# Optimization experiments

Measured on AMD Instinct MI355X. Metric: run time of the kernel, lower is better.

## Reference

```python
import jax, jax.numpy as jnp
import numpy as np

B, N_STEPS, N_TUMBLES = 512, 20000, 64
RATE_01 = RATE_10 = RATE_02 = RATE_20 = 1e-3
SPEED_0, SPEED_1 = 1e-3, 5e-3
DT = 0.01
PA_MU, PA_SIG = 0.0, 0.1   # planar cauchy
NP_MU, NP_SIG = 0.0, 0.5   # nonplanar cauchy


def _normalise(v):
    return v / jnp.linalg.norm(v, axis=-1, keepdims=True)


def _orthogonalise(v, u):
    return v - (jnp.sum(v * u, -1, keepdims=True) / jnp.sum(u * u, -1, keepdims=True)) * u


def _cauchy_angles(u, mu, sigma):
    # inverse-CDF cauchy sample, nan/inf -> 0, fmod pi (matches torch semantics)
    a = mu + sigma * jnp.tan(np.pi * (u - 0.5))
    a = jnp.where(jnp.isfinite(a), a, 0.0)
    return jnp.fmod(a, np.pi)


def _skew(u):  # (B,3) -> (B,3,3), [u]_x
    z = jnp.zeros_like(u[:, 0])
    return jnp.stack([
        jnp.stack([z, -u[:, 2], u[:, 1]], -1),
        jnp.stack([u[:, 2], z, -u[:, 0]], -1),
        jnp.stack([-u[:, 1], u[:, 0], z], -1)], -2)


def _rodrigues(u, ang):  # rotation about unit axis u by ang, per batch
    I = jnp.eye(3, dtype=u.dtype)
    c = jnp.cos(ang)[:, None, None]
    s = jnp.sin(ang)[:, None, None]
    return c * I + s * _skew(u) + (1.0 - c) * jnp.einsum('bi,bj->bij', u, u)


def setup_inputs() -> dict:
    key = jax.random.key(0)
    k = jax.random.split(key, 6)
    return {
        'x0': jnp.zeros((B, 3), jnp.float32),
        'v0': jax.random.uniform(k[0], (B, 3), jnp.float32),
        'v1': jax.random.uniform(k[1], (B, 3), jnp.float32),
        'r0': jax.random.uniform(k[2], (B, N_STEPS), jnp.float32),
        'r1': jax.random.uniform(k[3], (B, N_STEPS), jnp.float32),
        'u_planar': jax.random.uniform(k[4], (B, N_TUMBLES), jnp.float32),
        'u_nonplanar': jax.random.uniform(k[5], (B, N_TUMBLES), jnp.float32),
        'T': 200,
    }


def reference(x0, v0, v1, r0, r1, u_planar, u_nonplanar, T):
    b, n_steps = r0.shape

    # ---- three-state Markov chain over time (sequential) ----
    def state_step(s, rt):
        r0t, r1t = rt
        from0 = jnp.where(r0t < RATE_01, 1, jnp.where(r0t > 1.0 - RATE_02, 2, 0))
        from1 = jnp.where(r1t < RATE_10, 0, 1)
        from2 = jnp.where(r1t < RATE_20, 0, 1)
        ns = jnp.where(s == 0, from0, jnp.where(s == 1, from1, from2))
        return ns, ns

    s0 = jnp.zeros((b,), jnp.int32)
    _, states_t = jax.lax.scan(state_step, s0, (r0.T, r1.T))
    states = states_t.T  # (B, n_steps)

    # ---- initial orthonormal frame ----
    e0 = _normalise(v0)
    e1 = _normalise(_orthogonalise(v1, e0))
    e2 = _normalise(jnp.cross(e0, e1))

    # ---- tumble rotations (sequential over tumble events) ----
    pa = _cauchy_angles(u_planar, PA_MU, PA_SIG)      # (B, cap)
    npa = _cauchy_angles(u_nonplanar, NP_MU, NP_SIG)  # (B, cap)

    def rot_step(frames, angs):
        e0, e1, e2 = frames
        a_p, a_n = angs
        Rp = _rodrigues(e2, a_p)  # planar: rotate about e2
        e0 = _normalise(jnp.einsum('bij,bj->bi', Rp, e0))
        e1 = _normalise(jnp.einsum('bij,bj->bi', Rp, e1))
        e1 = _normalise(_orthogonalise(e1, e0))
        e2 = _normalise(jnp.cross(e0, e1))
        Rn = _rodrigues(e1, a_n)  # nonplanar: rotate about e1
        e0 = _normalise(jnp.einsum('bij,bj->bi', Rn, e0))
        e1 = _normalise(_orthogonalise(e1, e0))
        e2 = _normalise(jnp.cross(e0, e1))
        return (e0, e1, e2), e0

    _, e0_hist = jax.lax.scan(rot_step, (e0, e1, e2), (pa.T, npa.T))
    e0s = jnp.concatenate([e0[:, None, :], jnp.transpose(e0_hist, (1, 0, 2))], axis=1)  # (B, cap+1, 3)

    # ---- trajectory: per-step velocity = active frame * speed(state), 0 during tumbles ----
    tumble = (states == 2).at[:, 0].set(False)  # loop in original starts at step 1
    c = jnp.cumsum(tumble.astype(jnp.int32), axis=1)
    # original: k=0; at each tumble e0=e0s[:,k]; k+=1 => after m tumbles active frame is e0s[:, max(m-1,0)]
    idx = jnp.clip(c - 1, 0, pa.shape[1])
    frames = jnp.take_along_axis(e0s, idx[..., None], axis=1)  # (B, n_steps, 3)
    speed = jnp.where(states == 1, SPEED_1, SPEED_0).astype(frames.dtype)[..., None]
    vel = jnp.where(tumble[..., None], 0.0, frames * speed)
    vel = vel.at[:, 0, :].set(x0)  # e0_exp[:,0] = x
    X = jnp.cumsum(vel, axis=1)  # (B, n_steps, 3)
    return X
```

## Files before the change

### kernel.cpp

```cpp
#include <hip/hip_runtime.h>
#include <math.h>
#include <stdint.h>

#define NB 512
#define NT 20000
#define CAP 64
#define CHUNK 100
#define NC 200
#define NWORDS ((NB * NT) / 32)

static_assert(CHUNK * NC == NT, "chunking must cover all steps");
static_assert((NB * NT) % 64 == 0, "pack wave alignment");
static_assert(NT % 32 == 0, "b*NT word-aligned");

#define PI_F 3.14159265358979323846f

__device__ __forceinline__ float3 f3(float x, float y, float z) { return make_float3(x, y, z); }

__device__ __forceinline__ float3 norm3(float3 v) {
    float n = sqrtf(v.x * v.x + v.y * v.y + v.z * v.z);
    return f3(v.x / n, v.y / n, v.z / n);
}
__device__ __forceinline__ float3 cross3(float3 a, float3 b) {
    return f3(a.y * b.z - a.z * b.y, a.z * b.x - a.x * b.z, a.x * b.y - a.y * b.x);
}
__device__ __forceinline__ float dot3(float3 a, float3 b) { return a.x * b.x + a.y * b.y + a.z * b.z; }
__device__ __forceinline__ float3 orth3(float3 v, float3 u) {
    float d = dot3(v, u) / dot3(u, u);
    return f3(v.x - d * u.x, v.y - d * u.y, v.z - d * u.z);
}
__device__ __forceinline__ float3 rotv(float3 u, float c, float s, float3 v) {
    float3 cv = cross3(u, v);
    float du = dot3(u, v) * (1.0f - c);
    return f3(c * v.x + s * cv.x + du * u.x,
              c * v.y + s * cv.y + du * u.y,
              c * v.z + s * cv.z + du * u.z);
}

__device__ __forceinline__ float cauchy_ang(float u, float sigma) {
    float x = PI_F * (u - 0.5f);
    float t = (float)tan((double)x);
    float a = sigma * t;
    if (!isfinite(a)) a = 0.0f;
    return fmodf(a, PI_F);
}

__global__ __launch_bounds__(256) void k_angles(const float* __restrict__ up, const float* __restrict__ un,
                                                float* __restrict__ trig) {
    int tid = blockIdx.x * 256 + threadIdx.x;
    int k = tid >> 9, b = tid & (NB - 1);
    float ap = cauchy_ang(up[b * CAP + k], 0.1f);
    float an = cauchy_ang(un[b * CAP + k], 0.5f);
    ((float4*)trig)[tid] = make_float4(cosf(ap), sinf(ap), cosf(an), sinf(an));
}

__global__ __launch_bounds__(64) void k_chain(const float* __restrict__ v0, const float* __restrict__ v1,
                                              const float* __restrict__ trig, float* __restrict__ e0s) {
    int b = blockIdx.x * 64 + threadIdx.x;
    if (b >= NB) return;
    float3 a0 = f3(v0[b * 3], v0[b * 3 + 1], v0[b * 3 + 2]);
    float3 a1 = f3(v1[b * 3], v1[b * 3 + 1], v1[b * 3 + 2]);
    float3 e0 = norm3(a0);
    float3 e1 = norm3(orth3(a1, e0));
    float3 e2 = norm3(cross3(e0, e1));
    float* o = e0s + (size_t)b * (CAP + 1) * 3;
    o[0] = e0.x; o[1] = e0.y; o[2] = e0.z;
    for (int k = 0; k < CAP; k++) {
        float4 t4 = ((const float4*)trig)[k * NB + b];
        float cp = t4.x, sp = t4.y, cn = t4.z, sn = t4.w;
        float3 e0r = rotv(e2, cp, sp, e0);
        float3 e1r = rotv(e2, cp, sp, e1);
        e0 = norm3(e0r);
        e1 = norm3(e1r);
        e1 = norm3(orth3(e1, e0));
        e2 = norm3(cross3(e0, e1));
        e0 = norm3(rotv(e1, cn, sn, e0));
        e1 = norm3(orth3(e1, e0));
        e2 = norm3(cross3(e0, e1));
        o[(k + 1) * 3] = e0.x; o[(k + 1) * 3 + 1] = e0.y; o[(k + 1) * 3 + 2] = e0.z;
    }
}

__global__ __launch_bounds__(256) void k_pack(const float* __restrict__ r0, const float* __restrict__ r1,
                                              uint32_t* __restrict__ p0, uint32_t* __restrict__ p1,
                                              uint32_t* __restrict__ pf) {
    int g = blockIdx.x * 256 + threadIdx.x;
    float a = r0[g], d = r1[g];
    int f0 = (a < 1e-3f) ? 1 : ((a > (1.0f - 1e-3f)) ? 2 : 0);
    int f1 = (d < 1e-3f) ? 0 : 1;
    uint64_t b0 = __ballot(f0 & 1);
    uint64_t b1 = __ballot((f0 >> 1) & 1);
    uint64_t bf = __ballot(f1);
    if ((threadIdx.x & 63) == 0) {
        int w = g >> 6;
        ((uint64_t*)p0)[w] = b0;
        ((uint64_t*)p1)[w] = b1;
        ((uint64_t*)pf)[w] = bf;
    }
}

__device__ __forceinline__ void load100(const uint32_t* __restrict__ p, int w0, int off, uint32_t r[4]) {
    uint32_t q0 = p[w0], q1 = p[w0 + 1], q2 = p[w0 + 2], q3 = p[w0 + 3], q4 = p[w0 + 4];
    r[0] = __builtin_amdgcn_alignbit(q1, q0, off);
    r[1] = __builtin_amdgcn_alignbit(q2, q1, off);
    r[2] = __builtin_amdgcn_alignbit(q3, q2, off);
    r[3] = __builtin_amdgcn_alignbit(q4, q3, off);
}

#define GETB(R, t) ((R[(t) >> 5] >> ((t) & 31)) & 1u)

__global__ __launch_bounds__(512) void k_summary(const uint32_t* __restrict__ p0, const uint32_t* __restrict__ p1,
                                                 const uint32_t* __restrict__ pf, uint32_t* __restrict__ comb) {
    int c = blockIdx.x, b = threadIdx.x;
    int g0 = b * NT + c * CHUNK;
    uint32_t R0[4], R1[4], RF[4];
    load100(p0, g0 >> 5, g0 & 31, R0);
    load100(p1, g0 >> 5, g0 & 31, R1);
    load100(pf, g0 >> 5, g0 & 31, RF);
    int s0 = 0, s1 = 1, s2 = 2, c0 = 0, c1 = 0, c2 = 0;
#pragma unroll
    for (int t = 0; t < CHUNK; t++) {
        int f0 = (int)(GETB(R0, t) | (GETB(R1, t) << 1));
        int f1 = (int)GETB(RF, t);
        s0 = (s0 == 0) ? f0 : f1;
        s1 = (s1 == 0) ? f0 : f1;
        s2 = (s2 == 0) ? f0 : f1;
        bool skip = (c == 0) && (t == 0);
        c0 += (s0 == 2 && !skip);
        c1 += (s1 == 2 && !skip);
        c2 += (s2 == 2 && !skip);
    }
    comb[c * NB + b] = (uint32_t)(s0 | (s1 << 2) | (s2 << 4) | (c0 << 8) | (c1 << 16) | (c2 << 24));
}

__global__ void k_scan_state(const uint32_t* __restrict__ comb, uint32_t* __restrict__ entry) {
    int b = blockIdx.x * blockDim.x + threadIdx.x;
    if (b >= NB) return;
    uint32_t s = 0, C = 0;
#pragma unroll 4
    for (int c = 0; c < NC; c++) {
        uint32_t m = comb[c * NB + b];
        entry[c * NB + b] = s | (C << 2);
        C += (m >> (8 + 8 * s)) & 0xFF;
        s = (m >> (2 * s)) & 3;
    }
}

template <int MODE>
__global__ __launch_bounds__(256) void k_walk(const uint32_t* __restrict__ p0, const uint32_t* __restrict__ p1,
                                              const uint32_t* __restrict__ pf,
                                              const float* __restrict__ x0, const float* __restrict__ e0s,
                                              const uint32_t* __restrict__ entry,
                                              const float* __restrict__ epos,
                                              float* __restrict__ cvel, float* __restrict__ out) {
    __shared__ float se[(CAP + 1) * 3];
    int b = blockIdx.x, c = threadIdx.x;
    for (int i = threadIdx.x; i < (CAP + 1) * 3; i += blockDim.x)
        se[i] = e0s[(size_t)b * (CAP + 1) * 3 + i];
    __syncthreads();
    if (c >= NC) return;
    int g0 = b * NT + c * CHUNK;
    uint32_t R0[4], R1[4], RF[4];
    load100(p0, g0 >> 5, g0 & 31, R0);
    load100(p1, g0 >> 5, g0 & 31, R1);
    load100(pf, g0 >> 5, g0 & 31, RF);
    uint32_t e = entry[c * NB + b];
    int s = (int)(e & 3);
    int C = (int)(e >> 2);
    float px = 0.f, py = 0.f, pz = 0.f;
    if (MODE == 1) {
        const float* pp = epos + (size_t)(c * NB + b) * 3;
        px = pp[0]; py = pp[1]; pz = pp[2];
    }
    float* op = out + (size_t)(b * NT + c * CHUNK) * 3;
#pragma unroll
    for (int t = 0; t < CHUNK; t++) {
        int f0 = (int)(GETB(R0, t) | (GETB(R1, t) << 1));
        int f1 = (int)GETB(RF, t);
        s = (s == 0) ? f0 : f1;
        float vx, vy, vz;
        if (c == 0 && t == 0) {
            vx = x0[b * 3]; vy = x0[b * 3 + 1]; vz = x0[b * 3 + 2];
        } else if (s == 2) {
            C++;
            vx = 0.f; vy = 0.f; vz = 0.f;
        } else {
            int idx = C - 1;
            idx = idx < 0 ? 0 : (idx > CAP ? CAP : idx);
            float spd = (s == 1) ? 5e-3f : 1e-3f;
            vx = se[idx * 3] * spd; vy = se[idx * 3 + 1] * spd; vz = se[idx * 3 + 2] * spd;
        }
        px += vx; py += vy; pz += vz;
        if (MODE == 1) {
            op[t * 3] = px; op[t * 3 + 1] = py; op[t * 3 + 2] = pz;
        }
    }
    if (MODE == 0) {
        float* cv = cvel + (size_t)(c * NB + b) * 3;
        cv[0] = px; cv[1] = py; cv[2] = pz;
    }
}

__global__ void k_scan_pos(const float* __restrict__ cvel, float* __restrict__ epos) {
    int b = blockIdx.x * blockDim.x + threadIdx.x;
    if (b >= NB) return;
    float px = 0.f, py = 0.f, pz = 0.f;
#pragma unroll 4
    for (int c = 0; c < NC; c++) {
        float* ep = epos + (size_t)(c * NB + b) * 3;
        ep[0] = px; ep[1] = py; ep[2] = pz;
        const float* cv = cvel + (size_t)(c * NB + b) * 3;
        px += cv[0]; py += cv[1]; pz += cv[2];
    }
}

extern "C" void kernel_launch(void* const* d_in, const int* in_sizes, int n_in,
                              void* d_out, int out_size, void* d_ws, size_t ws_size,
                              hipStream_t stream) {
    const float* x0 = (const float*)d_in[0];
    const float* v0 = (const float*)d_in[1];
    const float* v1 = (const float*)d_in[2];
    const float* r0 = (const float*)d_in[3];
    const float* r1 = (const float*)d_in[4];
    const float* up = (const float*)d_in[5];
    const float* un = (const float*)d_in[6];
    float* out = (float*)d_out;

    char* w = (char*)d_ws;
    float* trig = (float*)w;       w += (size_t)NB * CAP * 4 * sizeof(float);
    float* e0s = (float*)w;        w += (size_t)NB * (CAP + 1) * 3 * sizeof(float);
    uint32_t* p0 = (uint32_t*)w;   w += (size_t)(NWORDS + 16) * 4;
    uint32_t* p1 = (uint32_t*)w;   w += (size_t)(NWORDS + 16) * 4;
    uint32_t* pf = (uint32_t*)w;   w += (size_t)(NWORDS + 16) * 4;
    uint32_t* comb = (uint32_t*)w; w += (size_t)NC * NB * 4;
    uint32_t* entry = (uint32_t*)w; w += (size_t)NC * NB * 4;
    float* cvel = (float*)w;       w += (size_t)NC * NB * 3 * sizeof(float);
    float* epos = (float*)w;       w += (size_t)NC * NB * 3 * sizeof(float);

    k_angles<<<dim3(NB * CAP / 256), dim3(256), 0, stream>>>(up, un, trig);
    k_chain<<<dim3(NB / 64), dim3(64), 0, stream>>>(v0, v1, trig, e0s);
    k_pack<<<dim3(NB * NT / 256), dim3(256), 0, stream>>>(r0, r1, p0, p1, pf);
    k_summary<<<dim3(NC), dim3(NB), 0, stream>>>(p0, p1, pf, comb);
    k_scan_state<<<dim3(2), dim3(256), 0, stream>>>(comb, entry);
    k_walk<0><<<dim3(NB), dim3(256), 0, stream>>>(p0, p1, pf, x0, e0s, entry, nullptr, cvel, nullptr);
    k_scan_pos<<<dim3(2), dim3(256), 0, stream>>>(cvel, epos);
    k_walk<1><<<dim3(NB), dim3(256), 0, stream>>>(p0, p1, pf, x0, e0s, entry, epos, nullptr, out);
}
```

Baseline: 401.5 us.

## Fuse pack, state scan, and position scan into one per-row kernel

Replaces the six-kernel pipeline (bit-packing, chunk summaries, serial state scan, two walks, serial position scan) with a single kernel that has one block per batch row. Each block packs the flags into shared memory and computes the three-state chunk summaries. It then runs Hillis-Steele scans in shared memory for state/count composition and for partial positions. Output writes are vectorised as float4 per four steps. This removes kernel launches, global round-trips and the slow single-thread serial scans over chunks. The cost is block-level barriers and a recomputation pass, and it changes the chunk size to 80.

```diff
diff --git a/kernel.cpp b/kernel.cpp
--- a/kernel.cpp
+++ b/kernel.cpp
@@ -5,13 +5,12 @@
 #define NB 512
 #define NT 20000
 #define CAP 64
-#define CHUNK 100
-#define NC 200
-#define NWORDS ((NB * NT) / 32)
+#define CHUNK 80
+#define NC 250
+#define CPAD 21
 
 static_assert(CHUNK * NC == NT, "chunking must cover all steps");
-static_assert((NB * NT) % 64 == 0, "pack wave alignment");
-static_assert(NT % 32 == 0, "b*NT word-aligned");
+static_assert(CHUNK % 4 == 0, "byte-packing needs 4 | CHUNK");
 
 #define PI_F 3.14159265358979323846f
 
@@ -81,136 +80,186 @@
     }
 }
 
-__global__ __launch_bounds__(256) void k_pack(const float* __restrict__ r0, const float* __restrict__ r1,
-                                              uint32_t* __restrict__ p0, uint32_t* __restrict__ p1,
-                                              uint32_t* __restrict__ pf) {
-    int g = blockIdx.x * 256 + threadIdx.x;
-    float a = r0[g], d = r1[g];
-    int f0 = (a < 1e-3f) ? 1 : ((a > (1.0f - 1e-3f)) ? 2 : 0);
-    int f1 = (d < 1e-3f) ? 0 : 1;
-    uint64_t b0 = __ballot(f0 & 1);
-    uint64_t b1 = __ballot((f0 >> 1) & 1);
-    uint64_t bf = __ballot(f1);
-    if ((threadIdx.x & 63) == 0) {
-        int w = g >> 6;
-        ((uint64_t*)p0)[w] = b0;
-        ((uint64_t*)p1)[w] = b1;
-        ((uint64_t*)pf)[w] = bf;
-    }
-}
-
-__device__ __forceinline__ void load100(const uint32_t* __restrict__ p, int w0, int off, uint32_t r[4]) {
-    uint32_t q0 = p[w0], q1 = p[w0 + 1], q2 = p[w0 + 2], q3 = p[w0 + 3], q4 = p[w0 + 4];
-    r[0] = __builtin_amdgcn_alignbit(q1, q0, off);
-    r[1] = __builtin_amdgcn_alignbit(q2, q1, off);
-    r[2] = __builtin_amdgcn_alignbit(q3, q2, off);
-    r[3] = __builtin_amdgcn_alignbit(q4, q3, off);
-}
-
-#define GETB(R, t) ((R[(t) >> 5] >> ((t) & 31)) & 1u)
-
-__global__ __launch_bounds__(512) void k_summary(const uint32_t* __restrict__ p0, const uint32_t* __restrict__ p1,
-                                                 const uint32_t* __restrict__ pf, uint32_t* __restrict__ comb) {
-    int c = blockIdx.x, b = threadIdx.x;
-    int g0 = b * NT + c * CHUNK;
-    uint32_t R0[4], R1[4], RF[4];
-    load100(p0, g0 >> 5, g0 & 31, R0);
-    load100(p1, g0 >> 5, g0 & 31, R1);
-    load100(pf, g0 >> 5, g0 & 31, RF);
-    int s0 = 0, s1 = 1, s2 = 2, c0 = 0, c1 = 0, c2 = 0;
-#pragma unroll
-    for (int t = 0; t < CHUNK; t++) {
-        int f0 = (int)(GETB(R0, t) | (GETB(R1, t) << 1));
-        int f1 = (int)GETB(RF, t);
-        s0 = (s0 == 0) ? f0 : f1;
-        s1 = (s1 == 0) ? f0 : f1;
-        s2 = (s2 == 0) ? f0 : f1;
-        bool skip = (c == 0) && (t == 0);
-        c0 += (s0 == 2 && !skip);
-        c1 += (s1 == 2 && !skip);
-        c2 += (s2 == 2 && !skip);
-    }
-    comb[c * NB + b] = (uint32_t)(s0 | (s1 << 2) | (s2 << 4) | (c0 << 8) | (c1 << 16) | (c2 << 24));
-}
-
-__global__ void k_scan_state(const uint32_t* __restrict__ comb, uint32_t* __restrict__ entry) {
-    int b = blockIdx.x * blockDim.x + threadIdx.x;
-    if (b >= NB) return;
-    uint32_t s = 0, C = 0;
-#pragma unroll 4
-    for (int c = 0; c < NC; c++) {
-        uint32_t m = comb[c * NB + b];
-        entry[c * NB + b] = s | (C << 2);
-        C += (m >> (8 + 8 * s)) & 0xFF;
-        s = (m >> (2 * s)) & 3;
-    }
-}
-
-template <int MODE>
-__global__ __launch_bounds__(256) void k_walk(const uint32_t* __restrict__ p0, const uint32_t* __restrict__ p1,
-                                              const uint32_t* __restrict__ pf,
-                                              const float* __restrict__ x0, const float* __restrict__ e0s,
-                                              const uint32_t* __restrict__ entry,
-                                              const float* __restrict__ epos,
-                                              float* __restrict__ cvel, float* __restrict__ out) {
+__device__ __forceinline__ uint4 comb2(uint4 A, uint4 B) {
+    uint4 R;
+    R.x = 0;
+    {
+        unsigned ms = A.x & 3u;
+        unsigned mf = (B.x >> (2u * ms)) & 3u;
+        R.x |= mf;
+        unsigned cB = (ms == 0u) ? B.y : ((ms == 1u) ? B.z : B.w);
+        R.y = A.y + cB;
+    }
+    {
+        unsigned ms = (A.x >> 2) & 3u;
+        unsigned mf = (B.x >> (2u * ms)) & 3u;
+        R.x |= mf << 2;
+        unsigned cB = (ms == 0u) ? B.y : ((ms == 1u) ? B.z : B.w);
+        R.z = A.z + cB;
+    }
+    {
+        unsigned ms = (A.x >> 4) & 3u;
+        unsigned mf = (B.x >> (2u * ms)) & 3u;
+        R.x |= mf << 4;
+        unsigned cB = (ms == 0u) ? B.y : ((ms == 1u) ? B.z : B.w);
+        R.w = A.w + cB;
+    }
+    return R;
+}
+
+#define DECODE(dw, t, f0, f1)                                        \
+    {                                                                \
+        uint32_t by_ = (dw[(t) >> 2] >> (((t) & 3) * 8)) & 0xFFu;    \
+        f0 = (int)(by_ & 3u);                                        \
+        f1 = (int)((by_ >> 2) & 1u);                                 \
+    }
+
+__global__ __launch_bounds__(256) void k_row(const float* __restrict__ r0, const float* __restrict__ r1,
+                                             const float* __restrict__ x0, const float* __restrict__ e0s,
+                                             float* __restrict__ out) {
+    __shared__ uint32_t dec[NC * CPAD];
     __shared__ float se[(CAP + 1) * 3];
-    int b = blockIdx.x, c = threadIdx.x;
-    for (int i = threadIdx.x; i < (CAP + 1) * 3; i += blockDim.x)
+    __shared__ uint4 S[NC];
+    __shared__ float Px[NC], Py[NC], Pz[NC];
+
+    int b = blockIdx.x, tid = threadIdx.x;
+
+    for (int i = tid; i < (CAP + 1) * 3; i += 256)
         se[i] = e0s[(size_t)b * (CAP + 1) * 3 + i];
+
+    const float4* q0 = (const float4*)(r0 + (size_t)b * NT);
+    const float4* q1 = (const float4*)(r1 + (size_t)b * NT);
+    for (int T = tid; T < NT / 4; T += 256) {
+        float4 a = q0[T], d = q1[T];
+        float ra[4] = {a.x, a.y, a.z, a.w};
+        float rd[4] = {d.x, d.y, d.z, d.w};
+        uint32_t w = 0;
+#pragma unroll
+        for (int j = 0; j < 4; j++) {
+            int f0 = (ra[j] < 1e-3f) ? 1 : ((ra[j] > (1.0f - 1e-3f)) ? 2 : 0);
+            int f1 = (rd[j] < 1e-3f) ? 0 : 1;
+            w |= (uint32_t)(f0 | (f1 << 2)) << (8 * j);
+        }
+        int t0 = T * 4;
+        int c = t0 / CHUNK;
+        int o = t0 - c * CHUNK;
+        dec[c * CPAD + (o >> 2)] = w;
+    }
     __syncthreads();
-    if (c >= NC) return;
-    int g0 = b * NT + c * CHUNK;
-    uint32_t R0[4], R1[4], RF[4];
-    load100(p0, g0 >> 5, g0 & 31, R0);
-    load100(p1, g0 >> 5, g0 & 31, R1);
-    load100(pf, g0 >> 5, g0 & 31, RF);
-    uint32_t e = entry[c * NB + b];
-    int s = (int)(e & 3);
-    int C = (int)(e >> 2);
-    float px = 0.f, py = 0.f, pz = 0.f;
-    if (MODE == 1) {
-        const float* pp = epos + (size_t)(c * NB + b) * 3;
-        px = pp[0]; py = pp[1]; pz = pp[2];
-    }
-    float* op = out + (size_t)(b * NT + c * CHUNK) * 3;
-#pragma unroll
-    for (int t = 0; t < CHUNK; t++) {
-        int f0 = (int)(GETB(R0, t) | (GETB(R1, t) << 1));
-        int f1 = (int)GETB(RF, t);
-        s = (s == 0) ? f0 : f1;
-        float vx, vy, vz;
-        if (c == 0 && t == 0) {
-            vx = x0[b * 3]; vy = x0[b * 3 + 1]; vz = x0[b * 3 + 2];
-        } else if (s == 2) {
-            C++;
-            vx = 0.f; vy = 0.f; vz = 0.f;
-        } else {
-            int idx = C - 1;
-            idx = idx < 0 ? 0 : (idx > CAP ? CAP : idx);
-            float spd = (s == 1) ? 5e-3f : 1e-3f;
-            vx = se[idx * 3] * spd; vy = se[idx * 3 + 1] * spd; vz = se[idx * 3 + 2] * spd;
-        }
-        px += vx; py += vy; pz += vz;
-        if (MODE == 1) {
-            op[t * 3] = px; op[t * 3 + 1] = py; op[t * 3 + 2] = pz;
-        }
-    }
-    if (MODE == 0) {
-        float* cv = cvel + (size_t)(c * NB + b) * 3;
-        cv[0] = px; cv[1] = py; cv[2] = pz;
-    }
-}
-
-__global__ void k_scan_pos(const float* __restrict__ cvel, float* __restrict__ epos) {
-    int b = blockIdx.x * blockDim.x + threadIdx.x;
-    if (b >= NB) return;
-    float px = 0.f, py = 0.f, pz = 0.f;
-#pragma unroll 4
-    for (int c = 0; c < NC; c++) {
-        float* ep = epos + (size_t)(c * NB + b) * 3;
-        ep[0] = px; ep[1] = py; ep[2] = pz;
-        const float* cv = cvel + (size_t)(c * NB + b) * 3;
-        px += cv[0]; py += cv[1]; pz += cv[2];
+
+    int c = tid;
+    uint32_t dw[CHUNK / 4];
+    if (c < NC) {
+#pragma unroll
+        for (int wi = 0; wi < CHUNK / 4; wi++) dw[wi] = dec[c * CPAD + wi];
+        int s0 = 0, s1 = 1, s2 = 2, c0 = 0, c1 = 0, c2 = 0;
+#pragma unroll
+        for (int t = 0; t < CHUNK; t++) {
+            int f0, f1;
+            DECODE(dw, t, f0, f1);
+            s0 = (s0 == 0) ? f0 : f1;
+            s1 = (s1 == 0) ? f0 : f1;
+            s2 = (s2 == 0) ? f0 : f1;
+            bool skip = (c == 0) && (t == 0);
+            c0 += (s0 == 2 && !skip);
+            c1 += (s1 == 2 && !skip);
+            c2 += (s2 == 2 && !skip);
+        }
+        S[c] = make_uint4((unsigned)(s0 | (s1 << 2) | (s2 << 4)),
+                          (unsigned)c0, (unsigned)c1, (unsigned)c2);
+    }
+    __syncthreads();
+
+    for (int off = 1; off < NC; off <<= 1) {
+        uint4 prev;
+        bool act = (c < NC) && (c >= off);
+        if (act) prev = S[c - off];
+        __syncthreads();
+        if (act) S[c] = comb2(prev, S[c]);
+        __syncthreads();
+    }
+
+    int es = 0;
+    uint32_t eC = 0;
+    if (c > 0 && c < NC) {
+        uint4 E = S[c - 1];
+        es = (int)(E.x & 3u);
+        eC = E.y;
+    }
+
+    float xx0 = x0[b * 3], xy0 = x0[b * 3 + 1], xz0 = x0[b * 3 + 2];
+
+    if (c < NC) {
+        int s = es;
+        uint32_t C = eC;
+        float px = 0.f, py = 0.f, pz = 0.f;
+#pragma unroll
+        for (int t = 0; t < CHUNK; t++) {
+            int f0, f1;
+            DECODE(dw, t, f0, f1);
+            s = (s == 0) ? f0 : f1;
+            float vx, vy, vz;
+            if (c == 0 && t == 0) {
+                vx = xx0; vy = xy0; vz = xz0;
+            } else if (s == 2) {
+                C++;
+                vx = 0.f; vy = 0.f; vz = 0.f;
+            } else {
+                int idx = (int)C - 1;
+                idx = idx < 0 ? 0 : (idx > CAP ? CAP : idx);
+                float spd = (s == 1) ? 5e-3f : 1e-3f;
+                vx = se[idx * 3] * spd; vy = se[idx * 3 + 1] * spd; vz = se[idx * 3 + 2] * spd;
+            }
+            px += vx; py += vy; pz += vz;
+        }
+        Px[c] = px; Py[c] = py; Pz[c] = pz;
+    }
+    __syncthreads();
+
+    for (int off = 1; off < NC; off <<= 1) {
+        float ax, ay, az;
+        bool act = (c < NC) && (c >= off);
+        if (act) { ax = Px[c - off]; ay = Py[c - off]; az = Pz[c - off]; }
+        __syncthreads();
+        if (act) { Px[c] += ax; Py[c] += ay; Pz[c] += az; }
+        __syncthreads();
+    }
+
+    if (c < NC) {
+        float px = 0.f, py = 0.f, pz = 0.f;
+        if (c > 0) { px = Px[c - 1]; py = Py[c - 1]; pz = Pz[c - 1]; }
+        int s = es;
+        uint32_t C = eC;
+        float* op = out + ((size_t)b * NT + (size_t)c * CHUNK) * 3;
+#pragma unroll
+        for (int g = 0; g < CHUNK / 4; g++) {
+            float buf[12];
+#pragma unroll
+            for (int j = 0; j < 4; j++) {
+                int t = g * 4 + j;
+                int f0, f1;
+                DECODE(dw, t, f0, f1);
+                s = (s == 0) ? f0 : f1;
+                float vx, vy, vz;
+                if (c == 0 && t == 0) {
+                    vx = xx0; vy = xy0; vz = xz0;
+                } else if (s == 2) {
+                    C++;
+                    vx = 0.f; vy = 0.f; vz = 0.f;
+                } else {
+                    int idx = (int)C - 1;
+                    idx = idx < 0 ? 0 : (idx > CAP ? CAP : idx);
+                    float spd = (s == 1) ? 5e-3f : 1e-3f;
+                    vx = se[idx * 3] * spd; vy = se[idx * 3 + 1] * spd; vz = se[idx * 3 + 2] * spd;
+                }
+                px += vx; py += vy; pz += vz;
+                buf[j * 3] = px; buf[j * 3 + 1] = py; buf[j * 3 + 2] = pz;
+            }
+            float4* o4 = (float4*)(op + g * 12);
+            o4[0] = make_float4(buf[0], buf[1], buf[2], buf[3]);
+            o4[1] = make_float4(buf[4], buf[5], buf[6], buf[7]);
+            o4[2] = make_float4(buf[8], buf[9], buf[10], buf[11]);
+        }
     }
 }
 
@@ -227,22 +276,10 @@
     float* out = (float*)d_out;
 
     char* w = (char*)d_ws;
-    float* trig = (float*)w;       w += (size_t)NB * CAP * 4 * sizeof(float);
-    float* e0s = (float*)w;        w += (size_t)NB * (CAP + 1) * 3 * sizeof(float);
-    uint32_t* p0 = (uint32_t*)w;   w += (size_t)(NWORDS + 16) * 4;
-    uint32_t* p1 = (uint32_t*)w;   w += (size_t)(NWORDS + 16) * 4;
-    uint32_t* pf = (uint32_t*)w;   w += (size_t)(NWORDS + 16) * 4;
-    uint32_t* comb = (uint32_t*)w; w += (size_t)NC * NB * 4;
-    uint32_t* entry = (uint32_t*)w; w += (size_t)NC * NB * 4;
-    float* cvel = (float*)w;       w += (size_t)NC * NB * 3 * sizeof(float);
-    float* epos = (float*)w;       w += (size_t)NC * NB * 3 * sizeof(float);
+    float* trig = (float*)w;  w += (size_t)NB * CAP * 4 * sizeof(float);
+    float* e0s = (float*)w;   w += (size_t)NB * (CAP + 1) * 3 * sizeof(float);
 
     k_angles<<<dim3(NB * CAP / 256), dim3(256), 0, stream>>>(up, un, trig);
     k_chain<<<dim3(NB / 64), dim3(64), 0, stream>>>(v0, v1, trig, e0s);
-    k_pack<<<dim3(NB * NT / 256), dim3(256), 0, stream>>>(r0, r1, p0, p1, pf);
-    k_summary<<<dim3(NC), dim3(NB), 0, stream>>>(p0, p1, pf, comb);
-    k_scan_state<<<dim3(2), dim3(256), 0, stream>>>(comb, entry);
-    k_walk<0><<<dim3(NB), dim3(256), 0, stream>>>(p0, p1, pf, x0, e0s, entry, nullptr, cvel, nullptr);
-    k_scan_pos<<<dim3(2), dim3(256), 0, stream>>>(cvel, epos);
-    k_walk<1><<<dim3(NB), dim3(256), 0, stream>>>(p0, p1, pf, x0, e0s, entry, epos, nullptr, out);
-}
+    k_row<<<dim3(NB), dim3(256), 0, stream>>>(r0, r1, x0, e0s, out);
+}
```

After: 352.6 us. 1.14x faster.
